# Kernel tuning notes

Hardware: AMD Instinct MI355X
Metric: run time of the kernel (lower is better)

## Reference

```python
import jax, jax.numpy as jnp
import numpy as np

N_USER, N_ITEM, N_KNOW, HIDDEN, BATCH = 200000, 20000, 128, 256, 16384
N_EDGES = 2 * N_KNOW - 3  # chain edges (k-1,k) k=1..K-1 then skip edges (k-2,k) k=2..K-1


def setup_inputs() -> dict:
    key = jax.random.key(0)
    ks = jax.random.split(key, 12)
    return {
        'user_ids': jax.random.randint(ks[0], (BATCH,), 0, N_USER),
        'item_ids': jax.random.randint(ks[1], (BATCH,), 0, N_ITEM),
        'item_know': (jax.random.uniform(ks[2], (BATCH, N_KNOW)) < 0.5).astype(jnp.float32),
        'priori': jax.random.normal(ks[3], (N_USER, N_KNOW), jnp.float32),
        'condi_p': jax.random.normal(ks[4], (N_USER, N_EDGES), jnp.float32),
        'condi_n': jax.random.normal(ks[5], (N_USER, N_EDGES), jnp.float32),
        'item_diff_w': jax.random.normal(ks[6], (N_ITEM, N_KNOW), jnp.float32),
        'item_disc_w': jax.random.normal(ks[7], (N_ITEM, 1), jnp.float32),
        'Wu': jax.random.normal(ks[8], (HIDDEN, N_KNOW), jnp.float32) * 0.05,
        'bu': jax.random.normal(ks[9], (HIDDEN,), jnp.float32) * 0.05,
        'Wi': jax.random.normal(ks[10], (HIDDEN, N_KNOW), jnp.float32) * 0.05,
        'bi': jax.random.normal(ks[11], (HIDDEN,), jnp.float32) * 0.05,
    }


def _posterior(bp, bcp, bcn):
    # bp: [B,K] sigmoid(priori rows); bcp/bcn: [B,E] sigmoid(condi rows).
    # Topological DAG propagation. For node k the torch code sums over all
    # 2^len_p predecessor bitmasks of prod_j(mask_j*margin_p_j + (1-mask_j)*margin_n_j),
    # which factorizes exactly to prod_j(margin_p_j + margin_n_j) (same math).
    K = bp.shape[1]
    p0 = bp[:, 0]                               # node 0: no predecessors
    p1 = bcp[:, 0] * p0 + bcn[:, 0] * (1.0 - p0)  # node 1: pred {0}, exponent 1/1
    # nodes k>=2 have sorted preds {k-2, k-1}; edge (k-1,k) -> col k-1, edge (k-2,k) -> col (K-1)+(k-2)
    cp_b, cn_b = bcp[:, 1:K - 1].T, bcn[:, 1:K - 1].T      # (k-1,k) edges, [K-2,B]
    cp_a, cn_a = bcp[:, K - 1:].T, bcn[:, K - 1:].T        # (k-2,k) edges, [K-2,B]

    def step(carry, x):
        p_km2, p_km1 = carry
        cpa, cna, cpb, cnb = x
        # pow(condi, 1/len_p) with len_p=2 -> sqrt
        ta = jnp.sqrt(cpa) * p_km2 + jnp.sqrt(cna) * (1.0 - p_km2)
        tb = jnp.sqrt(cpb) * p_km1 + jnp.sqrt(cnb) * (1.0 - p_km1)
        pk = ta * tb
        return (p_km1, pk), pk

    _, rest = jax.lax.scan(step, (p0, p1), (cp_a, cn_a, cp_b, cn_b))  # rest: [K-2,B]
    return jnp.concatenate([p0[:, None], p1[:, None], rest.T], axis=1)  # [B,K]


def reference(user_ids, item_ids, item_know, priori, condi_p, condi_n,
              item_diff_w, item_disc_w, Wu, bu, Wi, bi):
    bp = jax.nn.sigmoid(priori[user_ids])      # [B,K]
    bcp = jax.nn.sigmoid(condi_p[user_ids])    # [B,E]
    bcn = jax.nn.sigmoid(condi_n[user_ids])
    mastery = _posterior(bp, bcp, bcn)         # [B,K]
    idiff = jax.nn.sigmoid(item_diff_w[item_ids])  # [B,K]
    idisc = jax.nn.sigmoid(item_disc_w[item_ids])  # [B,1]
    user_factor = jnp.tanh((mastery * item_know) @ Wu.T + bu)      # [B,H]
    item_factor = jax.nn.sigmoid((idiff * item_know) @ Wi.T + bi)  # [B,H]
    # mirt2pl: 1/(1+exp(-sum(u*i) + offset)) == sigmoid(sum - offset)
    logits = jnp.sum(user_factor * item_factor, axis=1, keepdims=True) - idisc
    return jax.nn.sigmoid(logits)  # [B,1]
```

## Files before the change

### kernel.cpp

```cpp
#include <hip/hip_runtime.h>
#include <hip/hip_fp16.h>

#define BATCH   16384
#define NKNOW   128
#define NEDGE   253
#define RPB     16

typedef __attribute__((ext_vector_type(8))) short  s16x8;
typedef __attribute__((ext_vector_type(4))) float  f32x4;
typedef __attribute__((ext_vector_type(4))) int    i32x4;

typedef unsigned short u16;
typedef unsigned int   u32;
typedef unsigned long long u64;

__device__ __forceinline__ float sigm(float x) { return 1.0f / (1.0f + __expf(-x)); }

__device__ __forceinline__ u16 f2bf_rn(float x) {
    u32 u = __float_as_uint(x);
    u += 0x7FFFu + ((u >> 16) & 1u);
    return (u16)(u >> 16);
}
__device__ __forceinline__ float bf2f(u16 h) { return __uint_as_float(((u32)h) << 16); }

__device__ __forceinline__ u16 f2hc(float x) {
    __half h = __float2half_rn(x - 0.5f);
    u16 v; __builtin_memcpy(&v, &h, 2); return v;
}
__device__ __forceinline__ float h2fc(u32 u) {
    u16 v = (u16)u; __half h; __builtin_memcpy(&h, &v, 2);
    return __half2float(h);
}

__device__ __forceinline__ int swz(int row, int kbyte) {
    return row * 256 + (kbyte ^ ((row & 7) << 4));
}
__device__ __forceinline__ void store_pair(char* Mh, char* Ml, int r, int k0, float va, float vb) {
    int off = swz(r, k0 * 2);
    u16 ha = f2bf_rn(va); u16 la = f2bf_rn(va - bf2f(ha));
    u16 hb = f2bf_rn(vb); u16 lb = f2bf_rn(vb - bf2f(hb));
    *(u32*)(Mh + off) = (u32)ha | ((u32)hb << 16);
    *(u32*)(Ml + off) = (u32)la | ((u32)lb << 16);
}

__global__ __launch_bounds__(256, 4) void gather_ncd(
    const int*   __restrict__ user_ids,
    const float* __restrict__ priori,
    const float* __restrict__ condi_p,
    const float* __restrict__ condi_n,
    const float* __restrict__ Wu,
    const float* __restrict__ Wi,
    u16*         __restrict__ wsp,
    uint2*       __restrict__ cbT16)
{
    __shared__ float4 stage[4][128];

    const int wid = threadIdx.x >> 6, j = threadIdx.x & 63;
    const int r0  = blockIdx.x * 4;
    const int row = r0 + wid;
    const int uid = user_ids[row];
    const float* cp = condi_p + (size_t)uid * NEDGE;
    const float* cn = condi_n + (size_t)uid * NEDGE;

    float a0p = cp[127 + j], a0n = cn[127 + j], b0p = cp[1 + j], b0n = cn[1 + j];
    float a1p = 0.f, a1n = 0.f, b1p = 0.f, b1n = 0.f;
    if (j < 62) { a1p = cp[191 + j]; a1n = cn[191 + j]; b1p = cp[65 + j]; b1n = cn[65 + j]; }
    float c0p = cp[0], c0n = cn[0], pri = priori[(size_t)uid * NKNOW];

    float4 sA;
    sA.x = sqrtf(sigm(a0p)); sA.y = sqrtf(sigm(a0n));
    sA.z = sqrtf(sigm(b0p)); sA.w = sqrtf(sigm(b0n));
    stage[wid][1 + j] = sA;
    if (j < 62) {
        float4 sB;
        sB.x = sqrtf(sigm(a1p)); sB.y = sqrtf(sigm(a1n));
        sB.z = sqrtf(sigm(b1p)); sB.w = sqrtf(sigm(b1n));
        stage[wid][65 + j] = sB;
    }
    if (j == 0) {
        float4 h; h.x = sigm(c0p); h.y = sigm(c0n); h.z = sigm(pri); h.w = 0.5f;
        stage[wid][0] = h;
    }
    __syncthreads();

    for (int idx = threadIdx.x; idx < 4 * 127; idx += 256) {
        const int slot = idx >> 2, rr = idx & 3;
        float4 v = stage[rr][slot];
        uint2 o;
        o.x = (u32)f2hc(v.x) | ((u32)f2hc(v.y) << 16);
        o.y = (u32)f2hc(v.z) | ((u32)f2hc(v.w) << 16);
        cbT16[(size_t)slot * BATCH + r0 + rr] = o;
    }

    if (blockIdx.x < 256) {
        int i = blockIdx.x * 256 + threadIdx.x;
        bool isU = i < 32768;
        int  jj  = isU ? i : i - 32768;
        float w  = isU ? Wu[jj] : Wi[jj];
        u16 h = f2bf_rn(w);
        u16 l = f2bf_rn(w - bf2f(h));
        int base = isU ? 0 : 65536;
        wsp[base + jj]         = h;
        wsp[base + 32768 + jj] = l;
    }
}

__global__ __launch_bounds__(256, 2) void cg_ncd(
    const int*   __restrict__ item_ids,
    const float* __restrict__ item_know,
    const float* __restrict__ item_diff_w,
    const float* __restrict__ item_disc_w,
    const float* __restrict__ bu,
    const float* __restrict__ bi,
    const u16*   __restrict__ wsp,
    const uint2* __restrict__ cbT16,
    float*       __restrict__ out)
{
    __shared__ __align__(16) u16 sMh[32 * 128];
    __shared__ __align__(16) u16 sMl[32 * 128];
    __shared__ __align__(16) u16 sDh[32 * 128];
    __shared__ __align__(16) u16 sDl[32 * 128];
    __shared__ __align__(16) u16 sKm[32 * 128];
    __shared__ float sRed[4][32];
    __shared__ float sDisc[32];

    const int tid  = threadIdx.x;
    const int lane = tid & 63;
    const int wid  = tid >> 6;
    const int l15  = lane & 15, lq = lane >> 4;
    const int r0   = blockIdx.x * 32;

    if (wid == 0) {
        if (lane < 32) {
            const int r = lane;
            const uint2* base = cbT16 + (r0 + r);
            uint2 hh = base[0];
            float c0p = h2fc(hh.x) + 0.5f;
            float c0n = h2fc(hh.x >> 16) + 0.5f;
            float p0  = h2fc(hh.y) + 0.5f;
            float p1  = fmaf(p0, c0p - c0n, c0n);
            store_pair((char*)sMh, (char*)sMl, r, 0, p0, p1);

            float pm2 = p0, pm1 = p1, pev = 0.f;
            uint2 A[14], Bv[14];
#define LOADB(buf, bi_)                                               \
    _Pragma("unroll")                                                 \
    for (int t = 0; t < 14; ++t)                                      \
        buf[t] = base[(size_t)(1 + 14 * (bi_) + t) * BATCH];
#define STEPS(buf, bi_)                                               \
    _Pragma("unroll")                                                 \
    for (int t = 0; t < 14; ++t) {                                    \
        const int k = 2 + 14 * (bi_) + t;                             \
        uint2 sv = buf[t];                                            \
        float ax = h2fc(sv.x), ay = h2fc(sv.x >> 16);                 \
        float bx = h2fc(sv.y), by = h2fc(sv.y >> 16);                 \
        float ta = fmaf(pm2, ax - ay, ay + 0.5f);                     \
        float tb = fmaf(pm1, bx - by, by + 0.5f);                     \
        float pk = ta * tb;                                           \
        if (k & 1) store_pair((char*)sMh, (char*)sMl, r, k - 1, pev, pk); \
        else       pev = pk;                                          \
        pm2 = pm1; pm1 = pk;                                          \
    }
            LOADB(A, 0);
            LOADB(Bv, 1); STEPS(A, 0);
            LOADB(A, 2);  STEPS(Bv, 1);
            LOADB(Bv, 3); STEPS(A, 2);
            LOADB(A, 4);  STEPS(Bv, 3);
            LOADB(Bv, 5); STEPS(A, 4);
            LOADB(A, 6);  STEPS(Bv, 5);
            LOADB(Bv, 7); STEPS(A, 6);
            LOADB(A, 8);  STEPS(Bv, 7);
            STEPS(A, 8);
#undef LOADB
#undef STEPS
        } else {
            sDisc[lane - 32] = sigm(item_disc_w[item_ids[r0 + lane - 32]]);
        }
    } else if (wid <= 2) {
        const int rbase = (wid - 1) * 16;
        for (int rr = 0; rr < 16; ++rr) {
            const int r = rbase + rr, row = r0 + r;
            const int iid = item_ids[row];
            const float* kw = item_know   + (size_t)row * NKNOW;
            const float* dw = item_diff_w + (size_t)iid * NKNOW;
            #pragma unroll
            for (int half = 0; half < 2; ++half) {
                const int e = half * 64 + lane;
                float kv = kw[e];
                float dv = sigm(dw[e]) * kv;
                u16 dh = f2bf_rn(dv);
                u16 dl = f2bf_rn(dv - bf2f(dh));
                const int off = swz(r, 2 * e);
                *(u16*)((char*)sDh + off) = dh;
                *(u16*)((char*)sDl + off) = dl;
                *(u16*)((char*)sKm + off) = (kv > 0.5f) ? (u16)0xFFFFu : (u16)0;
            }
        }
    }
    __syncthreads();

    const u16* WuH = wsp;
    const u16* WuL = wsp + 32768;
    const u16* WiH = wsp + 65536;
    const u16* WiL = wsp + 98304;

    float rowsum[2][4] = {{0.f,0.f,0.f,0.f},{0.f,0.f,0.f,0.f}};

    #pragma unroll 1
    for (int t = 0; t < 4; ++t) {
        const int hcol = wid * 64 + t * 16 + l15;
        s16x8 uh[4], ul[4], ih[4], il[4];
        #pragma unroll
        for (int kc = 0; kc < 4; ++kc) {
            const int ke = kc * 32 + lq * 8;
            uh[kc] = *(const s16x8*)(WuH + hcol * NKNOW + ke);
            ul[kc] = *(const s16x8*)(WuL + hcol * NKNOW + ke);
            ih[kc] = *(const s16x8*)(WiH + hcol * NKNOW + ke);
            il[kc] = *(const s16x8*)(WiL + hcol * NKNOW + ke);
        }
        const float bub = bu[hcol], bib = bi[hcol];

        #pragma unroll
        for (int rg = 0; rg < 2; ++rg) {
            const int lr = rg * 16 + l15;
            f32x4 accU = {0.f, 0.f, 0.f, 0.f};
            f32x4 accV = {0.f, 0.f, 0.f, 0.f};
            #pragma unroll
            for (int kc = 0; kc < 4; ++kc) {
                const int offA = swz(lr, kc * 64 + lq * 16);
                i32x4 km = *(const i32x4*)((const char*)sKm + offA);
                i32x4 mh = *(const i32x4*)((const char*)sMh + offA) & km;
                i32x4 ml = *(const i32x4*)((const char*)sMl + offA) & km;
                s16x8 ah = *(s16x8*)&mh;
                s16x8 al = *(s16x8*)&ml;
                s16x8 dh = *(const s16x8*)((const char*)sDh + offA);
                s16x8 dl = *(const s16x8*)((const char*)sDl + offA);
                accU = __builtin_amdgcn_mfma_f32_16x16x32_bf16(ah, uh[kc], accU, 0, 0, 0);
                accU = __builtin_amdgcn_mfma_f32_16x16x32_bf16(ah, ul[kc], accU, 0, 0, 0);
                accU = __builtin_amdgcn_mfma_f32_16x16x32_bf16(al, uh[kc], accU, 0, 0, 0);
                accV = __builtin_amdgcn_mfma_f32_16x16x32_bf16(dh, ih[kc], accV, 0, 0, 0);
                accV = __builtin_amdgcn_mfma_f32_16x16x32_bf16(dh, il[kc], accV, 0, 0, 0);
                accV = __builtin_amdgcn_mfma_f32_16x16x32_bf16(dl, ih[kc], accV, 0, 0, 0);
            }
            #pragma unroll
            for (int j = 0; j < 4; ++j) {
                float x = accU[j] + bub;
                float u = 1.0f - 2.0f / (1.0f + __expf(2.0f * x));
                float v = sigm(accV[j] + bib);
                rowsum[rg][j] += u * v;
            }
        }
    }

    #pragma unroll
    for (int rg = 0; rg < 2; ++rg)
        #pragma unroll
        for (int j = 0; j < 4; ++j) {
            float v = rowsum[rg][j];
            v += __shfl_xor(v, 1);
            v += __shfl_xor(v, 2);
            v += __shfl_xor(v, 4);
            v += __shfl_xor(v, 8);
            if (l15 == 0) sRed[wid][rg * 16 + lq * 4 + j] = v;
        }
    __syncthreads();

    if (tid < 32) {
        float s = sRed[0][tid] + sRed[1][tid] + sRed[2][tid] + sRed[3][tid];
        out[r0 + tid] = sigm(s - sDisc[tid]);
    }
}

__global__ void conv_w(const float* __restrict__ Wu, const float* __restrict__ Wi,
                       u16* __restrict__ wsp) {
    int i = blockIdx.x * 256 + threadIdx.x;
    bool isU = i < 32768;
    int  j   = isU ? i : i - 32768;
    float w  = isU ? Wu[j] : Wi[j];
    u16 h = f2bf_rn(w);
    u16 l = f2bf_rn(w - bf2f(h));
    int base = isU ? 0 : 65536;
    wsp[base + j]         = h;
    wsp[base + 32768 + j] = l;
}

__global__ __launch_bounds__(256, 3) void fused_ncd(
    const int*   __restrict__ user_ids,
    const int*   __restrict__ item_ids,
    const float* __restrict__ item_know,
    const float* __restrict__ priori,
    const float* __restrict__ condi_p,
    const float* __restrict__ condi_n,
    const float* __restrict__ item_diff_w,
    const float* __restrict__ item_disc_w,
    const float* __restrict__ bu,
    const float* __restrict__ bi,
    const u16* __restrict__ wsp,
    float*       __restrict__ out)
{
    __shared__ float sPair[RPB][508];
    __shared__ __align__(16) u16 sMhi[RPB * 128];
    __shared__ __align__(16) u16 sMlo[RPB * 128];
    __shared__ __align__(16) u16 sDhi[RPB * 128];
    __shared__ __align__(16) u16 sDlo[RPB * 128];
    __shared__ __align__(16) u16 sKmF[RPB * 128];
    __shared__ float sRed[4][RPB];
    __shared__ float sDisc[RPB];

    const int tid  = threadIdx.x;
    const int lane = tid & 63;
    const int wid  = tid >> 6;
    const int r0   = blockIdx.x * RPB;

    for (int rr = 0; rr < 4; ++rr) {
        const int r   = wid * 4 + rr;
        const int row = r0 + r;
        const int uid = user_ids[row];
        const int iid = item_ids[row];
        const float* cp = condi_p + (size_t)uid * NEDGE;
        const float* cn = condi_n + (size_t)uid * NEDGE;
        for (int e = lane; e < NEDGE; e += 64) {
            float p = sigm(cp[e]);
            float n = sigm(cn[e]);
            if (e >= 1) { p = sqrtf(p); n = sqrtf(n); }
            *(float2*)&sPair[r][2 * e] = make_float2(p, n);
        }
        const float* dw = item_diff_w + (size_t)iid * NKNOW;
        const float* kw = item_know   + (size_t)row * NKNOW;
        for (int e = lane; e < NKNOW; e += 64) {
            float kv = kw[e];
            float dv = sigm(dw[e]) * kv;
            u16 dh = f2bf_rn(dv);
            u16 dl = f2bf_rn(dv - bf2f(dh));
            int off = swz(r, 2 * e);
            *(u16*)((char*)sDhi + off) = dh;
            *(u16*)((char*)sDlo + off) = dl;
            *(u16*)((char*)sKmF + off) = (kv > 0.5f) ? (u16)0xFFFFu : (u16)0;
        }
    }
    __syncthreads();

    if (tid < RPB) {
        const int r   = tid;
        const int row = r0 + r;
        const int uid = user_ids[row];
        const int iid = item_ids[row];
        const float* P = &sPair[r][0];
        float p0 = sigm(priori[(size_t)uid * NKNOW]);
        float2 c0 = *(const float2*)&P[0];
        float p1 = c0.x * p0 + c0.y * (1.0f - p0);
        store_pair((char*)sMhi, (char*)sMlo, r, 0, p0, p1);
        float pm2 = p0, pm1 = p1, pev = 0.0f;
        for (int k = 2; k < NKNOW; ++k) {
            float2 a = *(const float2*)&P[2 * (125 + k)];
            float2 b = *(const float2*)&P[2 * (k - 1)];
            float ta = fmaf(pm2, a.x - a.y, a.y);
            float tb = fmaf(pm1, b.x - b.y, b.y);
            float pk = ta * tb;
            if (k & 1) store_pair((char*)sMhi, (char*)sMlo, r, k - 1, pev, pk);
            else       pev = pk;
            pm2 = pm1; pm1 = pk;
        }
        sDisc[r] = sigm(item_disc_w[iid]);
    }
    __syncthreads();

    const int l15 = lane & 15, lq = lane >> 4;
    const u16* WuH = wsp;
    const u16* WuL = wsp + 32768;
    const u16* WiH = wsp + 65536;
    const u16* WiL = wsp + 98304;

    float rowsum[4] = {0.f, 0.f, 0.f, 0.f};

    for (int t = 0; t < 4; ++t) {
        const int hcol = wid * 64 + t * 16 + l15;
        f32x4 accU = {0.f, 0.f, 0.f, 0.f};
        f32x4 accV = {0.f, 0.f, 0.f, 0.f};
        const u16* wuh = WuH + hcol * NKNOW;
        const u16* wul = WuL + hcol * NKNOW;
        const u16* wih = WiH + hcol * NKNOW;
        const u16* wil = WiL + hcol * NKNOW;
        #pragma unroll
        for (int kc = 0; kc < 4; ++kc) {
            const int offA = swz(l15, kc * 64 + lq * 16);
            const int ke   = kc * 32 + lq * 8;
            i32x4 km = *(const i32x4*)((const char*)sKmF + offA);
            i32x4 mh = *(const i32x4*)((const char*)sMhi + offA) & km;
            i32x4 ml = *(const i32x4*)((const char*)sMlo + offA) & km;
            s16x8 ah = *(s16x8*)&mh;
            s16x8 al = *(s16x8*)&ml;
            s16x8 bh = *(const s16x8*)((const char*)sDhi + offA);
            s16x8 bl = *(const s16x8*)((const char*)sDlo + offA);
            s16x8 uh = *(const s16x8*)(wuh + ke);
            s16x8 ul = *(const s16x8*)(wul + ke);
            s16x8 ih = *(const s16x8*)(wih + ke);
            s16x8 il = *(const s16x8*)(wil + ke);
            accU = __builtin_amdgcn_mfma_f32_16x16x32_bf16(ah, uh, accU, 0, 0, 0);
            accU = __builtin_amdgcn_mfma_f32_16x16x32_bf16(ah, ul, accU, 0, 0, 0);
            accU = __builtin_amdgcn_mfma_f32_16x16x32_bf16(al, uh, accU, 0, 0, 0);
            accV = __builtin_amdgcn_mfma_f32_16x16x32_bf16(bh, ih, accV, 0, 0, 0);
            accV = __builtin_amdgcn_mfma_f32_16x16x32_bf16(bh, il, accV, 0, 0, 0);
            accV = __builtin_amdgcn_mfma_f32_16x16x32_bf16(bl, ih, accV, 0, 0, 0);
        }
        const float bub = bu[hcol], bib = bi[hcol];
        #pragma unroll
        for (int j = 0; j < 4; ++j) {
            float x = accU[j] + bub;
            float u = 1.0f - 2.0f / (1.0f + __expf(2.0f * x));
            float v = sigm(accV[j] + bib);
            rowsum[j] += u * v;
        }
    }

    #pragma unroll
    for (int j = 0; j < 4; ++j) {
        float v = rowsum[j];
        v += __shfl_xor(v, 1);
        v += __shfl_xor(v, 2);
        v += __shfl_xor(v, 4);
        v += __shfl_xor(v, 8);
        if (l15 == 0) sRed[wid][lq * 4 + j] = v;
    }
    __syncthreads();

    if (tid < RPB) {
        float logit = sRed[0][tid] + sRed[1][tid] + sRed[2][tid] + sRed[3][tid] - sDisc[tid];
        out[r0 + tid] = sigm(logit);
    }
}

extern "C" void kernel_launch(void* const* d_in, const int* in_sizes, int n_in,
                              void* d_out, int out_size, void* d_ws, size_t ws_size,
                              hipStream_t stream) {
    const int*   user_ids    = (const int*)  d_in[0];
    const int*   item_ids    = (const int*)  d_in[1];
    const float* item_know   = (const float*)d_in[2];
    const float* priori      = (const float*)d_in[3];
    const float* condi_p     = (const float*)d_in[4];
    const float* condi_n     = (const float*)d_in[5];
    const float* item_diff_w = (const float*)d_in[6];
    const float* item_disc_w = (const float*)d_in[7];
    const float* Wu          = (const float*)d_in[8];
    const float* bu          = (const float*)d_in[9];
    const float* Wi          = (const float*)d_in[10];
    const float* bi          = (const float*)d_in[11];
    float* out = (float*)d_out;

    char* base = (char*)d_ws;
    u16*   wsp   = (u16*)base;
    uint2* cbT16 = (uint2*)(base + 0x40000);
    const size_t need = 0x40000 + (size_t)127 * BATCH * 8;

    if (ws_size >= need) {
        gather_ncd<<<BATCH / 4, 256, 0, stream>>>(
            user_ids, priori, condi_p, condi_n, Wu, Wi, wsp, cbT16);
        cg_ncd<<<BATCH / 32, 256, 0, stream>>>(
            item_ids, item_know, item_diff_w, item_disc_w, bu, bi,
            wsp, cbT16, out);
    } else {
        conv_w<<<256, 256, 0, stream>>>(Wu, Wi, wsp);
        fused_ncd<<<BATCH / RPB, 256, 0, stream>>>(
            user_ids, item_ids, item_know, priori, condi_p, condi_n,
            item_diff_w, item_disc_w, bu, bi, wsp, out);
    }
}
```

Before: 48.66 us.

## Move item difficulty/knowledge preprocessing into gather kernel via workspace buffers

Moves the item_know and item_diff_w gather, the sigmoid, and the bf16 hi/lo split out of the cg_ncd producer warps and into the highly parallel gather_ncd kernel. That kernel writes packed u32 pairs to three workspace arrays, and cg_ncd then only copies them into swizzled shared memory. The aim is to shorten the serial prologue in cg_ncd, where two warps handled 16 rows each, by spreading the work across many more threads. The cost is an extra 12 MB of workspace traffic (write plus read) and a larger workspace requirement, which may send execution down the fallback path if the workspace is too small.

```diff
diff --git a/kernel.cpp b/kernel.cpp
--- a/kernel.cpp
+++ b/kernel.cpp
@@ -45,13 +45,19 @@
 
 __global__ __launch_bounds__(256, 4) void gather_ncd(
     const int*   __restrict__ user_ids,
+    const int*   __restrict__ item_ids,
+    const float* __restrict__ item_know,
     const float* __restrict__ priori,
     const float* __restrict__ condi_p,
     const float* __restrict__ condi_n,
+    const float* __restrict__ item_diff_w,
     const float* __restrict__ Wu,
     const float* __restrict__ Wi,
     u16*         __restrict__ wsp,
-    uint2*       __restrict__ cbT16)
+    uint2*       __restrict__ cbT16,
+    u32*         __restrict__ dhiw,
+    u32*         __restrict__ dlow,
+    u32*         __restrict__ kmw)
 {
     __shared__ float4 stage[4][128];
 
@@ -59,12 +65,17 @@
     const int r0  = blockIdx.x * 4;
     const int row = r0 + wid;
     const int uid = user_ids[row];
+    const int iid = item_ids[row];
     const float* cp = condi_p + (size_t)uid * NEDGE;
     const float* cn = condi_n + (size_t)uid * NEDGE;
+    const float* kw = item_know   + (size_t)row * NKNOW;
+    const float* dw = item_diff_w + (size_t)iid * NKNOW;
 
     float a0p = cp[127 + j], a0n = cn[127 + j], b0p = cp[1 + j], b0n = cn[1 + j];
     float a1p = 0.f, a1n = 0.f, b1p = 0.f, b1n = 0.f;
     if (j < 62) { a1p = cp[191 + j]; a1n = cn[191 + j]; b1p = cp[65 + j]; b1n = cn[65 + j]; }
+    float2 k2 = *(const float2*)&kw[2 * j];
+    float2 d2 = *(const float2*)&dw[2 * j];
     float c0p = cp[0], c0n = cn[0], pri = priori[(size_t)uid * NKNOW];
 
     float4 sA;
@@ -80,6 +91,16 @@
     if (j == 0) {
         float4 h; h.x = sigm(c0p); h.y = sigm(c0n); h.z = sigm(pri); h.w = 0.5f;
         stage[wid][0] = h;
+    }
+
+    {
+        float dv0 = sigm(d2.x) * k2.x, dv1 = sigm(d2.y) * k2.y;
+        u16 h0 = f2bf_rn(dv0), h1 = f2bf_rn(dv1);
+        u16 l0 = f2bf_rn(dv0 - bf2f(h0)), l1 = f2bf_rn(dv1 - bf2f(h1));
+        const size_t o = (size_t)row * 64 + j;
+        dhiw[o] = (u32)h0 | ((u32)h1 << 16);
+        dlow[o] = (u32)l0 | ((u32)l1 << 16);
+        kmw[o]  = ((k2.x > 0.5f) ? 0x0000FFFFu : 0u) | ((k2.y > 0.5f) ? 0xFFFF0000u : 0u);
     }
     __syncthreads();
 
@@ -107,13 +128,14 @@
 
 __global__ __launch_bounds__(256, 2) void cg_ncd(
     const int*   __restrict__ item_ids,
-    const float* __restrict__ item_know,
-    const float* __restrict__ item_diff_w,
     const float* __restrict__ item_disc_w,
     const float* __restrict__ bu,
     const float* __restrict__ bi,
     const u16*   __restrict__ wsp,
     const uint2* __restrict__ cbT16,
+    const u32*   __restrict__ dhiw,
+    const u32*   __restrict__ dlow,
+    const u32*   __restrict__ kmw,
     float*       __restrict__ out)
 {
     __shared__ __align__(16) u16 sMh[32 * 128];
@@ -178,23 +200,17 @@
         }
     } else if (wid <= 2) {
         const int rbase = (wid - 1) * 16;
+        #pragma unroll 4
         for (int rr = 0; rr < 16; ++rr) {
-            const int r = rbase + rr, row = r0 + r;
-            const int iid = item_ids[row];
-            const float* kw = item_know   + (size_t)row * NKNOW;
-            const float* dw = item_diff_w + (size_t)iid * NKNOW;
-            #pragma unroll
-            for (int half = 0; half < 2; ++half) {
-                const int e = half * 64 + lane;
-                float kv = kw[e];
-                float dv = sigm(dw[e]) * kv;
-                u16 dh = f2bf_rn(dv);
-                u16 dl = f2bf_rn(dv - bf2f(dh));
-                const int off = swz(r, 2 * e);
-                *(u16*)((char*)sDh + off) = dh;
-                *(u16*)((char*)sDl + off) = dl;
-                *(u16*)((char*)sKm + off) = (kv > 0.5f) ? (u16)0xFFFFu : (u16)0;
-            }
+            const int r = rbase + rr;
+            const size_t o = (size_t)(r0 + r) * 64 + lane;
+            u32 dh2 = dhiw[o];
+            u32 dl2 = dlow[o];
+            u32 km2 = kmw[o];
+            const int off = swz(r, 4 * lane);
+            *(u32*)((char*)sDh + off) = dh2;
+            *(u32*)((char*)sDl + off) = dl2;
+            *(u32*)((char*)sKm + off) = km2;
         }
     }
     __syncthreads();
@@ -450,14 +466,19 @@
     char* base = (char*)d_ws;
     u16*   wsp   = (u16*)base;
     uint2* cbT16 = (uint2*)(base + 0x40000);
-    const size_t need = 0x40000 + (size_t)127 * BATCH * 8;
+    const size_t cbBytes = (size_t)127 * BATCH * 8;
+    u32* dhiw = (u32*)(base + 0x40000 + cbBytes);
+    u32* dlow = (u32*)(base + 0x40000 + cbBytes + 0x400000);
+    u32* kmw  = (u32*)(base + 0x40000 + cbBytes + 0x800000);
+    const size_t need = 0x40000 + cbBytes + 0xC00000;
 
     if (ws_size >= need) {
         gather_ncd<<<BATCH / 4, 256, 0, stream>>>(
-            user_ids, priori, condi_p, condi_n, Wu, Wi, wsp, cbT16);
+            user_ids, item_ids, item_know, priori, condi_p, condi_n,
+            item_diff_w, Wu, Wi, wsp, cbT16, dhiw, dlow, kmw);
         cg_ncd<<<BATCH / 32, 256, 0, stream>>>(
-            item_ids, item_know, item_diff_w, item_disc_w, bu, bi,
-            wsp, cbT16, out);
+            item_ids, item_disc_w, bu, bi, wsp, cbT16,
+            dhiw, dlow, kmw, out);
     } else {
         conv_w<<<256, 256, 0, stream>>>(Wu, Wi, wsp);
         fused_ncd<<<BATCH / RPB, 256, 0, stream>>>(
```

Result: slower. 50.21 us (+3.2%).
